# Performance work log

Hardware: AMD Instinct MI355X
Metric: run time of the kernel (lower is better)

## Reference

```python
import jax, jax.numpy as jnp
import numpy as np
from jax import lax

MAX_ALPHA = 0.00015
MAX_BETA = 0.00015
NOISE_GRAIN = 0.05
LN_EPS = 1e-5


def gaussian_blur(x, ksize, sigma):
    # depthwise 2D gaussian blur, same padding; x: [B, C, H, W]
    r = ksize // 2
    g = jnp.exp(-(jnp.linspace(-r, r, ksize, dtype=x.dtype) ** 2) / (2.0 * sigma ** 2))
    g = g / g.sum()
    k2d = g[:, None] * g[None, :]                       # [k, k]
    C = x.shape[1]
    kernel = jnp.broadcast_to(k2d, (C, 1, ksize, ksize))  # OIHW, depthwise
    return lax.conv_general_dilated(
        x, kernel, window_strides=(1, 1), padding=[(r, r), (r, r)],
        feature_group_count=C, dimension_numbers=('NCHW', 'OIHW', 'NCHW'))


def setup_inputs() -> dict:
    key = jax.random.key(0)
    ks = jax.random.split(key, 8)
    B, C, H, W = 8, 3, 1024, 1024
    L, D = 1024, 512
    Dh = D // 4
    return {
        'x_bg': jax.random.uniform(ks[0], (B, C, H, W), dtype=jnp.float32),
        'bottleneck_feat': jax.random.normal(ks[1], (B, L, D), dtype=jnp.float32),
        'mask': jax.random.uniform(ks[2], (B, 1, H, W), dtype=jnp.float32),
        'noise': jax.random.normal(ks[3], (B, C, H, W), dtype=jnp.float32),
        'W1': jax.random.normal(ks[4], (D, Dh), dtype=jnp.float32) * (1.0 / np.sqrt(D)),
        'b1': jnp.zeros((Dh,), dtype=jnp.float32),
        'ln_g': jnp.ones((Dh,), dtype=jnp.float32),
        'ln_b': jnp.zeros((Dh,), dtype=jnp.float32),
        'W2': jax.random.normal(ks[5], (Dh, 2), dtype=jnp.float32) * 0.01,
        'b2': jnp.zeros((2,), dtype=jnp.float32),
    }


def reference(x_bg, bottleneck_feat, mask, noise, W1, b1, ln_g, ln_b, W2, b2):
    # param head on global-pooled bottleneck feature
    feat_global = bottleneck_feat.mean(axis=1)                 # [B, D]
    h = feat_global @ W1 + b1                                  # [B, D/4]
    mu = h.mean(axis=-1, keepdims=True)
    var = ((h - mu) ** 2).mean(axis=-1, keepdims=True)
    h = (h - mu) * lax.rsqrt(var + LN_EPS) * ln_g + ln_b
    h = jax.nn.relu(h)
    params = h @ W2 + b2                                       # [B, 2]
    alpha = jax.nn.sigmoid(params[:, 0])[:, None, None, None] * MAX_ALPHA
    beta = jax.nn.sigmoid(params[:, 1])[:, None, None, None] * MAX_BETA

    # synthesize
    variance = alpha * x_bg + beta
    sigma = jnp.sqrt(jnp.maximum(variance, 1e-7))
    n = gaussian_blur(noise, 7, NOISE_GRAIN) * 1.5
    mask_soft = gaussian_blur(mask, 21, 5.0)                   # [B,1,H,W] broadcast
    noisy_output = x_bg + n * sigma * mask_soft
    return noisy_output, alpha, beta
```

## Files before the change

kernel.cpp:

```cpp
#include <hip/hip_runtime.h>
#include <math.h>

#define B 8
#define C 3
#define H 1024
#define W 1024
#define L 1024
#define D 512
#define DH 128
#define NPIX (H * W)
#define NOISY_ELEMS (B * C * NPIX)
#define TH 16
#define RPB 8
#define LROW 1056

typedef float vf2 __attribute__((ext_vector_type(2)));
typedef float vf4 __attribute__((ext_vector_type(4)));
typedef unsigned short us4 __attribute__((ext_vector_type(4)));

struct BlurW { float w[21]; };

static __device__ __forceinline__ unsigned short f2bf(float f) {
    unsigned u = __float_as_uint(f);
    u += 0x7FFFu + ((u >> 16) & 1u);
    return (unsigned short)(u >> 16);
}

__global__ __launch_bounds__(256) void hblur_colsum_kernel(
        const float* __restrict__ mask, unsigned short* __restrict__ hmask,
        const float* __restrict__ feat, float* __restrict__ partial, BlurW kw) {
    int wgid = blockIdx.x;
    int t = threadIdx.x;
    __shared__ float Ls[RPB][LROW];

    if (wgid < 1024) {
        size_t row0 = (size_t)wgid * RPB;
        const float* src = mask + row0 * W;
        #pragma unroll
        for (int r = 0; r < RPB; ++r) {
            vf4 v = *((const vf4*)(src + (size_t)r * W) + t);
            *(vf4*)&Ls[r][12 + 4 * t] = v;
        }
        if (t < RPB * 10) {
            int r = t / 10, i = t - 10 * r;
            Ls[r][2 + i] = 0.f;
            Ls[r][12 + W + i] = 0.f;
        }
        __syncthreads();
        unsigned short* dst = hmask + row0 * W;
        #pragma unroll
        for (int r = 0; r < RPB; ++r) {
            float v[28];
            #pragma unroll
            for (int j = 0; j < 7; ++j) {
                vf4 q = *(const vf4*)&Ls[r][4 * t + 4 * j];
                v[4 * j] = q.x; v[4 * j + 1] = q.y; v[4 * j + 2] = q.z; v[4 * j + 3] = q.w;
            }
            us4 o;
            #pragma unroll
            for (int i = 0; i < 4; ++i) {
                float acc = 0.f;
                #pragma unroll
                for (int k = 0; k < 10; ++k)
                    acc = fmaf(kw.w[k], v[i + 2 + k] + v[i + 22 - k], acc);
                acc = fmaf(kw.w[10], v[i + 12], acc);
                o[i] = f2bf(acc);
            }
            *(us4*)(dst + (size_t)r * W + 4 * t) = o;
        }
    } else {
        int blk = wgid - 1024;
        int b = blk >> 5, chunk = blk & 31;
        int d4 = (t & 127) * 4;
        int half = t >> 7;
        const float* base = feat + (size_t)b * (L * D)
                          + (size_t)(chunk * 32 + half * 16) * D + d4;
        vf4 s = {0.f, 0.f, 0.f, 0.f};
        #pragma unroll
        for (int ll = 0; ll < 16; ++ll) {
            vf4 v = *(const vf4*)(base + (size_t)ll * D);
            s.x += v.x; s.y += v.y; s.z += v.z; s.w += v.w;
        }
        float* dst = partial + ((size_t)(b * 64 + chunk * 2 + half)) * 512 + d4;
        *(vf4*)dst = s;
    }
}

__global__ void head_kernel(const float* __restrict__ partial,
                            const float* __restrict__ W1, const float* __restrict__ b1,
                            const float* __restrict__ ln_g, const float* __restrict__ ln_b,
                            const float* __restrict__ W2, const float* __restrict__ b2,
                            float* __restrict__ ab, float* __restrict__ out_tail) {
    const int b = blockIdx.x;
    const int j = threadIdx.x;
    __shared__ float fm[D];
    __shared__ float red[DH];
    for (int d = j; d < D; d += DH) {
        float s = 0.f;
        const float* p = partial + (size_t)b * 64 * D + d;
        for (int c = 0; c < 64; ++c) s += p[c * D];
        fm[d] = s * (1.0f / (float)L);
    }
    __syncthreads();
    float h = b1[j];
    const vf4* fm4 = (const vf4*)fm;
    #pragma unroll 8
    for (int d4 = 0; d4 < D / 4; ++d4) {
        vf4 f = fm4[d4];
        h = fmaf(f.x, W1[(4 * d4 + 0) * DH + j], h);
        h = fmaf(f.y, W1[(4 * d4 + 1) * DH + j], h);
        h = fmaf(f.z, W1[(4 * d4 + 2) * DH + j], h);
        h = fmaf(f.w, W1[(4 * d4 + 3) * DH + j], h);
    }

    red[j] = h; __syncthreads();
    for (int s = 64; s > 0; s >>= 1) { if (j < s) red[j] += red[j + s]; __syncthreads(); }
    float mu = red[0] * (1.f / (float)DH);
    __syncthreads();
    float hc = h - mu;
    red[j] = hc * hc; __syncthreads();
    for (int s = 64; s > 0; s >>= 1) { if (j < s) red[j] += red[j + s]; __syncthreads(); }
    float var = red[0] * (1.f / (float)DH);
    __syncthreads();

    float hn = hc * rsqrtf(var + 1e-5f) * ln_g[j] + ln_b[j];
    hn = fmaxf(hn, 0.f);

    red[j] = hn * W2[j * 2 + 0]; __syncthreads();
    for (int s = 64; s > 0; s >>= 1) { if (j < s) red[j] += red[j + s]; __syncthreads(); }
    float p0 = red[0];
    __syncthreads();
    red[j] = hn * W2[j * 2 + 1]; __syncthreads();
    for (int s = 64; s > 0; s >>= 1) { if (j < s) red[j] += red[j + s]; __syncthreads(); }
    float p1 = red[0];

    if (j == 0) {
        float a  = 0.00015f / (1.f + expf(-(p0 + b2[0])));
        float be = 0.00015f / (1.f + expf(-(p1 + b2[1])));
        ab[b] = a; ab[8 + b] = be;
        out_tail[b] = a; out_tail[8 + b] = be;
    }
}

__global__ __launch_bounds__(256) void final_kernel(
        const float* __restrict__ x_bg, const float* __restrict__ noise,
        const unsigned short* __restrict__ hmask, const float* __restrict__ ab,
        float* __restrict__ out, BlurW kw) {
    int blk = blockIdx.x;
    int b   = blk >> 7;
    int rem = blk & 127;
    int s   = rem >> 1;
    int wj  = rem & 1;
    int h0  = s * TH;
    int t   = threadIdx.x;
    int x0  = wj * 512 + 2 * t;

    const unsigned short* hmb = hmask + (size_t)b * NPIX + x0;
    const vf2 zero2 = {0.f, 0.f};

    vf2 win[21];
    #pragma unroll
    for (int k = 0; k < 21; ++k) {
        int hy = h0 - 10 + k;
        if (hy >= 0 && hy < H) {
            unsigned u = *(const unsigned*)(hmb + (size_t)hy * W);
            win[k].x = __uint_as_float(u << 16);
            win[k].y = __uint_as_float(u & 0xFFFF0000u);
        } else win[k] = zero2;
    }

    float alpha = ab[b], beta = ab[8 + b];

    #pragma unroll
    for (int r = 0; r < TH; ++r) {
        float mx = 0.f, my = 0.f;
        #pragma unroll
        for (int k = 0; k < 10; ++k) {
            float wk = kw.w[k];
            vf2 v1 = win[(r + k) % 21];
            vf2 v2 = win[(r + 20 - k) % 21];
            mx = fmaf(wk, v1.x + v2.x, mx);
            my = fmaf(wk, v1.y + v2.y, my);
        }
        {
            vf2 vm = win[(r + 10) % 21];
            mx = fmaf(kw.w[10], vm.x, mx);
            my = fmaf(kw.w[10], vm.y, my);
        }
        int h = h0 + r;
        #pragma unroll
        for (int c = 0; c < C; ++c) {
            size_t idx = (((size_t)(b * C + c) * H) + h) * W + x0;
            vf2 x  = *(const vf2*)(x_bg + idx);
            vf2 nz = *(const vf2*)(noise + idx);
            vf2 o;
            float sgx = sqrtf(fmaxf(fmaf(alpha, x.x, beta), 1e-7f));
            float sgy = sqrtf(fmaxf(fmaf(alpha, x.y, beta), 1e-7f));
            o.x = fmaf(1.5f * nz.x * sgx, mx, x.x);
            o.y = fmaf(1.5f * nz.y * sgy, my, x.y);
            __builtin_nontemporal_store(o, (vf2*)(out + idx));
        }
        if (r < TH - 1) {
            int hy = h0 + r + 11;
            int slot = r % 21;
            if (hy < H) {
                unsigned u = *(const unsigned*)(hmb + (size_t)hy * W);
                win[slot].x = __uint_as_float(u << 16);
                win[slot].y = __uint_as_float(u & 0xFFFF0000u);
            } else win[slot] = zero2;
        }
    }
}

extern "C" void kernel_launch(void* const* d_in, const int* in_sizes, int n_in,
                              void* d_out, int out_size, void* d_ws, size_t ws_size,
                              hipStream_t stream) {
    const float* x_bg = (const float*)d_in[0];
    const float* feat = (const float*)d_in[1];
    const float* mask = (const float*)d_in[2];
    const float* noise = (const float*)d_in[3];
    const float* W1 = (const float*)d_in[4];
    const float* b1 = (const float*)d_in[5];
    const float* ln_g = (const float*)d_in[6];
    const float* ln_b = (const float*)d_in[7];
    const float* W2 = (const float*)d_in[8];
    const float* b2 = (const float*)d_in[9];
    float* out = (float*)d_out;

    float* ws_f = (float*)d_ws;
    float* partial = ws_f;
    float* ab = ws_f + 262144;
    unsigned short* hmask = (unsigned short*)(ws_f + 262144 + 64);

    BlurW kw;
    {
        double g[21], s = 0.0;
        for (int i = 0; i < 21; ++i) { double x = (double)(i - 10); g[i] = exp(-x * x / 50.0); s += g[i]; }
        for (int i = 0; i < 21; ++i) kw.w[i] = (float)(g[i] / s);
    }

    hblur_colsum_kernel<<<1024 + 256, 256, 0, stream>>>(mask, hmask, feat, partial, kw);
    head_kernel<<<B, 128, 0, stream>>>(partial, W1, b1, ln_g, ln_b, W2, b2,
                                       ab, out + NOISY_ELEMS);
    final_kernel<<<1024, 256, 0, stream>>>(x_bg, noise, hmask, ab, out, kw);
}
```

Measured before the change: 94.35 us.

## Fuse param head into producer via last-block atomic; taller rows per final block

The separate head kernel is folded into the producer kernel. A per-batch atomic counter lets the last column-sum block for each batch run the LayerNorm/MLP head, which removes one kernel launch but adds a memset. The final kernel now processes 32 rows per block with half as many blocks. Its vertical blur window becomes a shifting register array in a rolled loop instead of modular indexing in a fully unrolled loop. This trades fewer launches and less halo reloading for lower parallelism in the final pass (512 blocks) and possible register-shift overhead.

```diff
diff --git a/kernel.cpp b/kernel.cpp
--- a/kernel.cpp
+++ b/kernel.cpp
@@ -10,7 +10,7 @@
 #define DH 128
 #define NPIX (H * W)
 #define NOISY_ELEMS (B * C * NPIX)
-#define TH 16
+#define TH 32
 #define RPB 8
 #define LROW 1056
 
@@ -26,14 +26,19 @@
     return (unsigned short)(u >> 16);
 }
 
-__global__ __launch_bounds__(256) void hblur_colsum_kernel(
+__global__ __launch_bounds__(256) void produce_kernel(
         const float* __restrict__ mask, unsigned short* __restrict__ hmask,
-        const float* __restrict__ feat, float* __restrict__ partial, BlurW kw) {
+        const float* __restrict__ feat, float* __restrict__ partial,
+        int* __restrict__ counters,
+        const float* __restrict__ W1, const float* __restrict__ b1,
+        const float* __restrict__ ln_g, const float* __restrict__ ln_b,
+        const float* __restrict__ W2, const float* __restrict__ b2,
+        float* __restrict__ ab, float* __restrict__ out_tail, BlurW kw) {
     int wgid = blockIdx.x;
     int t = threadIdx.x;
-    __shared__ float Ls[RPB][LROW];
 
     if (wgid < 1024) {
+        __shared__ float Ls[RPB][LROW];
         size_t row0 = (size_t)wgid * RPB;
         const float* src = mask + row0 * W;
         #pragma unroll
@@ -68,11 +73,14 @@
             }
             *(us4*)(dst + (size_t)r * W + 4 * t) = o;
         }
-    } else {
-        int blk = wgid - 1024;
-        int b = blk >> 5, chunk = blk & 31;
-        int d4 = (t & 127) * 4;
-        int half = t >> 7;
+        return;
+    }
+
+    int blk = wgid - 1024;
+    int b = blk >> 5, chunk = blk & 31;
+    int d4 = (t & 127) * 4;
+    int half = t >> 7;
+    {
         const float* base = feat + (size_t)b * (L * D)
                           + (size_t)(chunk * 32 + half * 16) * D + d4;
         vf4 s = {0.f, 0.f, 0.f, 0.f};
@@ -81,60 +89,68 @@
             vf4 v = *(const vf4*)(base + (size_t)ll * D);
             s.x += v.x; s.y += v.y; s.z += v.z; s.w += v.w;
         }
-        float* dst = partial + ((size_t)(b * 64 + chunk * 2 + half)) * 512 + d4;
-        *(vf4*)dst = s;
-    }
-}
-
-__global__ void head_kernel(const float* __restrict__ partial,
-                            const float* __restrict__ W1, const float* __restrict__ b1,
-                            const float* __restrict__ ln_g, const float* __restrict__ ln_b,
-                            const float* __restrict__ W2, const float* __restrict__ b2,
-                            float* __restrict__ ab, float* __restrict__ out_tail) {
-    const int b = blockIdx.x;
-    const int j = threadIdx.x;
+        *(vf4*)(partial + ((size_t)(b * 64 + chunk * 2 + half)) * 512 + d4) = s;
+    }
+
+    __threadfence();
+    __shared__ int winner;
+    if (t == 0) winner = (atomicAdd(&counters[b], 1) == 31);
+    __syncthreads();
+    if (!winner) return;
+    __threadfence();
+
     __shared__ float fm[D];
     __shared__ float red[DH];
-    for (int d = j; d < D; d += DH) {
-        float s = 0.f;
-        const float* p = partial + (size_t)b * 64 * D + d;
-        for (int c = 0; c < 64; ++c) s += p[c * D];
-        fm[d] = s * (1.0f / (float)L);
-    }
-    __syncthreads();
-    float h = b1[j];
-    const vf4* fm4 = (const vf4*)fm;
-    #pragma unroll 8
-    for (int d4 = 0; d4 < D / 4; ++d4) {
-        vf4 f = fm4[d4];
-        h = fmaf(f.x, W1[(4 * d4 + 0) * DH + j], h);
-        h = fmaf(f.y, W1[(4 * d4 + 1) * DH + j], h);
-        h = fmaf(f.z, W1[(4 * d4 + 2) * DH + j], h);
-        h = fmaf(f.w, W1[(4 * d4 + 3) * DH + j], h);
-    }
-
-    red[j] = h; __syncthreads();
-    for (int s = 64; s > 0; s >>= 1) { if (j < s) red[j] += red[j + s]; __syncthreads(); }
+    for (int d = t; d < D; d += 256) {
+        float acc = 0.f;
+        const float* p = partial + (size_t)b * 64 * 512 + d;
+        for (int g = 0; g < 64; ++g) acc += p[g * 512];
+        fm[d] = acc * (1.0f / (float)L);
+    }
+    __syncthreads();
+    float h = 0.f;
+    if (t < DH) {
+        h = b1[t];
+        const vf4* fm4 = (const vf4*)fm;
+        #pragma unroll 8
+        for (int q = 0; q < D / 4; ++q) {
+            vf4 f = fm4[q];
+            h = fmaf(f.x, W1[(4 * q + 0) * DH + t], h);
+            h = fmaf(f.y, W1[(4 * q + 1) * DH + t], h);
+            h = fmaf(f.z, W1[(4 * q + 2) * DH + t], h);
+            h = fmaf(f.w, W1[(4 * q + 3) * DH + t], h);
+        }
+    }
+
+    if (t < DH) red[t] = h;
+    __syncthreads();
+    for (int st = 64; st > 0; st >>= 1) { if (t < st) red[t] += red[t + st]; __syncthreads(); }
     float mu = red[0] * (1.f / (float)DH);
     __syncthreads();
     float hc = h - mu;
-    red[j] = hc * hc; __syncthreads();
-    for (int s = 64; s > 0; s >>= 1) { if (j < s) red[j] += red[j + s]; __syncthreads(); }
+    if (t < DH) red[t] = hc * hc;
+    __syncthreads();
+    for (int st = 64; st > 0; st >>= 1) { if (t < st) red[t] += red[t + st]; __syncthreads(); }
     float var = red[0] * (1.f / (float)DH);
     __syncthreads();
 
-    float hn = hc * rsqrtf(var + 1e-5f) * ln_g[j] + ln_b[j];
-    hn = fmaxf(hn, 0.f);
-
-    red[j] = hn * W2[j * 2 + 0]; __syncthreads();
-    for (int s = 64; s > 0; s >>= 1) { if (j < s) red[j] += red[j + s]; __syncthreads(); }
+    float hn = 0.f;
+    if (t < DH) {
+        hn = hc * rsqrtf(var + 1e-5f) * ln_g[t] + ln_b[t];
+        hn = fmaxf(hn, 0.f);
+    }
+
+    if (t < DH) red[t] = hn * W2[t * 2 + 0];
+    __syncthreads();
+    for (int st = 64; st > 0; st >>= 1) { if (t < st) red[t] += red[t + st]; __syncthreads(); }
     float p0 = red[0];
     __syncthreads();
-    red[j] = hn * W2[j * 2 + 1]; __syncthreads();
-    for (int s = 64; s > 0; s >>= 1) { if (j < s) red[j] += red[j + s]; __syncthreads(); }
+    if (t < DH) red[t] = hn * W2[t * 2 + 1];
+    __syncthreads();
+    for (int st = 64; st > 0; st >>= 1) { if (t < st) red[t] += red[t + st]; __syncthreads(); }
     float p1 = red[0];
 
-    if (j == 0) {
+    if (t == 0) {
         float a  = 0.00015f / (1.f + expf(-(p0 + b2[0])));
         float be = 0.00015f / (1.f + expf(-(p1 + b2[1])));
         ab[b] = a; ab[8 + b] = be;
@@ -147,8 +163,8 @@
         const unsigned short* __restrict__ hmask, const float* __restrict__ ab,
         float* __restrict__ out, BlurW kw) {
     int blk = blockIdx.x;
-    int b   = blk >> 7;
-    int rem = blk & 127;
+    int b   = blk >> 6;
+    int rem = blk & 63;
     int s   = rem >> 1;
     int wj  = rem & 1;
     int h0  = s * TH;
@@ -162,7 +178,7 @@
     #pragma unroll
     for (int k = 0; k < 21; ++k) {
         int hy = h0 - 10 + k;
-        if (hy >= 0 && hy < H) {
+        if (hy >= 0) {
             unsigned u = *(const unsigned*)(hmb + (size_t)hy * W);
             win[k].x = __uint_as_float(u << 16);
             win[k].y = __uint_as_float(u & 0xFFFF0000u);
@@ -171,22 +187,17 @@
 
     float alpha = ab[b], beta = ab[8 + b];
 
-    #pragma unroll
     for (int r = 0; r < TH; ++r) {
         float mx = 0.f, my = 0.f;
         #pragma unroll
         for (int k = 0; k < 10; ++k) {
             float wk = kw.w[k];
-            vf2 v1 = win[(r + k) % 21];
-            vf2 v2 = win[(r + 20 - k) % 21];
-            mx = fmaf(wk, v1.x + v2.x, mx);
-            my = fmaf(wk, v1.y + v2.y, my);
-        }
-        {
-            vf2 vm = win[(r + 10) % 21];
-            mx = fmaf(kw.w[10], vm.x, mx);
-            my = fmaf(kw.w[10], vm.y, my);
-        }
+            mx = fmaf(wk, win[k].x + win[20 - k].x, mx);
+            my = fmaf(wk, win[k].y + win[20 - k].y, my);
+        }
+        mx = fmaf(kw.w[10], win[10].x, mx);
+        my = fmaf(kw.w[10], win[10].y, my);
+
         int h = h0 + r;
         #pragma unroll
         for (int c = 0; c < C; ++c) {
@@ -200,14 +211,16 @@
             o.y = fmaf(1.5f * nz.y * sgy, my, x.y);
             __builtin_nontemporal_store(o, (vf2*)(out + idx));
         }
-        if (r < TH - 1) {
-            int hy = h0 + r + 11;
-            int slot = r % 21;
+
+        #pragma unroll
+        for (int i = 0; i < 20; ++i) win[i] = win[i + 1];
+        {
+            int hy = h + 11;
             if (hy < H) {
                 unsigned u = *(const unsigned*)(hmb + (size_t)hy * W);
-                win[slot].x = __uint_as_float(u << 16);
-                win[slot].y = __uint_as_float(u & 0xFFFF0000u);
-            } else win[slot] = zero2;
+                win[20].x = __uint_as_float(u << 16);
+                win[20].y = __uint_as_float(u & 0xFFFF0000u);
+            } else win[20] = zero2;
         }
     }
 }
@@ -230,17 +243,19 @@
     float* ws_f = (float*)d_ws;
     float* partial = ws_f;
     float* ab = ws_f + 262144;
+    int* counters = (int*)(ws_f + 262144 + 32);
     unsigned short* hmask = (unsigned short*)(ws_f + 262144 + 64);
 
     BlurW kw;
     {
-        double g[21], s = 0.0;
-        for (int i = 0; i < 21; ++i) { double x = (double)(i - 10); g[i] = exp(-x * x / 50.0); s += g[i]; }
-        for (int i = 0; i < 21; ++i) kw.w[i] = (float)(g[i] / s);
-    }
-
-    hblur_colsum_kernel<<<1024 + 256, 256, 0, stream>>>(mask, hmask, feat, partial, kw);
-    head_kernel<<<B, 128, 0, stream>>>(partial, W1, b1, ln_g, ln_b, W2, b2,
-                                       ab, out + NOISY_ELEMS);
-    final_kernel<<<1024, 256, 0, stream>>>(x_bg, noise, hmask, ab, out, kw);
-}
+        double g[21], ssum = 0.0;
+        for (int i = 0; i < 21; ++i) { double x = (double)(i - 10); g[i] = exp(-x * x / 50.0); ssum += g[i]; }
+        for (int i = 0; i < 21; ++i) kw.w[i] = (float)(g[i] / ssum);
+    }
+
+    hipMemsetAsync(counters, 0, 8 * sizeof(int), stream);
+    produce_kernel<<<1024 + 256, 256, 0, stream>>>(mask, hmask, feat, partial,
+                                                   counters, W1, b1, ln_g, ln_b,
+                                                   W2, b2, ab, out + NOISY_ELEMS, kw);
+    final_kernel<<<512, 256, 0, stream>>>(x_bg, noise, hmask, ab, out, kw);
+}
```

Result: slower. 154.0 us (+63.2%).
